# Kernel optimization log

Hardware: AMD Instinct MI355X
Metric: run time of the kernel (lower is better)

The kernel has to match this reference:

```python
import jax, jax.numpy as jnp
import numpy as np

T, B, I, H = 1024, 64, 1024, 1024


def setup_inputs() -> dict:
    key = jax.random.key(0)
    ks = jax.random.split(key, 7)
    s = 1.0 / np.sqrt(H)  # uniform_(-sqrt(k), sqrt(k)) with k = 1/hidden_size
    return {
        "x": jax.random.normal(ks[0], (T, B, I), dtype=jnp.float32),
        "W_ih": jax.random.normal(ks[1], (4 * H, I), dtype=jnp.float32) * s,
        "W_hh": jax.random.normal(ks[2], (4 * H, H), dtype=jnp.float32) * s,
        "b_ih": jax.random.normal(ks[3], (4 * H,), dtype=jnp.float32) * s,
        "b_hh": jax.random.normal(ks[4], (4 * H,), dtype=jnp.float32) * s,
        "h0": jax.random.uniform(ks[5], (B, H), dtype=jnp.float32, minval=-s, maxval=s),
        "c0": jax.random.uniform(ks[6], (B, H), dtype=jnp.float32, minval=-s, maxval=s),
    }


def reference(x, W_ih, W_hh, b_ih, b_hh, h0, c0):
    # Precompute input projections for all timesteps in one big GEMM: [T,B,4H]
    x_proj = jnp.einsum("tbi,gi->tbg", x, W_ih) + b_ih + b_hh

    def step(carry, xp_t):
        h, c = carry
        gates = xp_t + h @ W_hh.T  # [B, 4H]
        i, f, g, o = jnp.split(gates, 4, axis=-1)  # torch LSTMCell gate order
        i = jax.nn.sigmoid(i)
        f = jax.nn.sigmoid(f)
        g = jnp.tanh(g)
        o = jax.nn.sigmoid(o)
        c_new = f * c + i * g
        h_new = o * jnp.tanh(c_new)
        return (h_new, c_new), h_new

    (h_T, c_T), out = jax.lax.scan(step, (h0, c0), x_proj)
    return out, h_T, c_T  # out: [T, B, H]
```

## Files before the change

### kernel.cpp

```cpp
#include <hip/hip_runtime.h>

typedef unsigned short u16;
typedef __attribute__((ext_vector_type(8))) __bf16 bf16x8;
typedef __attribute__((ext_vector_type(4))) float f32x4;

#define NWG 256
#define CHUNK 64
#define NCHUNK 16

__device__ __forceinline__ u16 f2b(float f) {
  union { float f; unsigned u; } v; v.f = f;
  unsigned r = (v.u + 0x7fffu + ((v.u >> 16) & 1u)) >> 16;
  return (u16)r;
}
__device__ __forceinline__ float b2f(u16 u) {
  union { unsigned u; float f; } v; v.u = ((unsigned)u) << 16;
  return v.f;
}
__device__ __forceinline__ float sig(float x) { return 1.0f / (1.0f + __expf(-x)); }
__device__ __forceinline__ float tanh_(float x) { return 2.0f / (1.0f + __expf(-2.0f * x)) - 1.0f; }

__global__ __launch_bounds__(256) void prep_kernel(
    const float* __restrict__ W_ih, const float* __restrict__ W_hh,
    const float* __restrict__ b_ih, const float* __restrict__ b_hh,
    const float* __restrict__ h0, const float* __restrict__ c0,
    u16* __restrict__ Wc, float* __restrict__ bias,
    u16* __restrict__ hbuf, float* __restrict__ cst)
{
  const int tid = threadIdx.x;
  const int blk = blockIdx.x;
  {
    const float4 a = *reinterpret_cast<const float4*>(W_ih + (size_t)blk * 1024 + tid * 4);
    const float4 b = *reinterpret_cast<const float4*>(W_hh + (size_t)blk * 1024 + tid * 4);
    u16* dst = Wc + (size_t)blk * 2048;
    *reinterpret_cast<ushort4*>(dst + tid * 4) =
        make_ushort4(f2b(a.x), f2b(a.y), f2b(a.z), f2b(a.w));
    *reinterpret_cast<ushort4*>(dst + 1024 + tid * 4) =
        make_ushort4(f2b(b.x), f2b(b.y), f2b(b.z), f2b(b.w));
  }
  if (blk < 16) {
    int i = blk * 256 + tid;
    bias[i] = b_ih[i] + b_hh[i];
  } else if (blk < 80) {
    int row = blk - 16, k = tid * 4;
    float4 v = *reinterpret_cast<const float4*>(h0 + (size_t)row * 1024 + k);
    *reinterpret_cast<ushort4*>(hbuf + (size_t)row * 1024 + k) =
        make_ushort4(f2b(v.x), f2b(v.y), f2b(v.z), f2b(v.w));
  } else if (blk < 144) {
    int row = blk - 80, k = tid * 4;
    *reinterpret_cast<float4*>(cst + (size_t)row * 1024 + k) =
        *reinterpret_cast<const float4*>(c0 + (size_t)row * 1024 + k);
  }
}

__global__ __launch_bounds__(256) void xproj_kernel(
    const float* __restrict__ xc, const u16* __restrict__ Wc, u16* __restrict__ Xp)
{
  __shared__ __align__(16) u16 As[128][72];
  __shared__ __align__(16) u16 Bs[128][72];
  const int tid = threadIdx.x;
  const int w = tid >> 6, l = tid & 63;
  const int bm = blockIdx.x & 31;
  const int bn = blockIdx.x >> 5;
  const int m0 = bm << 7, n0 = bn << 7;
  const int wm = w & 1, wn = w >> 1;
  const int lr = l & 15, lq = l >> 4;

  f32x4 acc[4][4];
  for (int i = 0; i < 4; ++i)
    for (int j = 0; j < 4; ++j) acc[i][j] = (f32x4){0.f, 0.f, 0.f, 0.f};

  for (int kc = 0; kc < 1024; kc += 64) {
    {
      const int k4 = (tid & 15) << 2;
      const int rb = tid >> 4;
      for (int rp = 0; rp < 128; rp += 16) {
        int row = rp + rb;
        float4 v = *reinterpret_cast<const float4*>(xc + (size_t)(m0 + row) * 1024 + kc + k4);
        unsigned lo = (unsigned)f2b(v.x) | ((unsigned)f2b(v.y) << 16);
        unsigned hi = (unsigned)f2b(v.z) | ((unsigned)f2b(v.w) << 16);
        *reinterpret_cast<uint2*>(&As[row][k4]) = make_uint2(lo, hi);
      }
    }
    {
      const int kk = (tid & 7) << 3;
      const int rb = tid >> 3;
      for (int rp = 0; rp < 128; rp += 32) {
        int row = rp + rb;
        uint4 v = *reinterpret_cast<const uint4*>(Wc + (size_t)(n0 + row) * 2048 + kc + kk);
        *reinterpret_cast<uint4*>(&Bs[row][kk]) = v;
      }
    }
    __syncthreads();
    for (int kb = 0; kb < 2; ++kb) {
      const int ko = kb * 32 + lq * 8;
      bf16x8 af[4], bfr[4];
      for (int i = 0; i < 4; ++i)
        af[i] = *reinterpret_cast<const bf16x8*>(&As[(wm << 6) + (i << 4) + lr][ko]);
      for (int j = 0; j < 4; ++j)
        bfr[j] = *reinterpret_cast<const bf16x8*>(&Bs[(wn << 6) + (j << 4) + lr][ko]);
      for (int i = 0; i < 4; ++i)
        for (int j = 0; j < 4; ++j)
          acc[i][j] = __builtin_amdgcn_mfma_f32_16x16x32_bf16(af[i], bfr[j], acc[i][j], 0, 0, 0);
    }
    __syncthreads();
  }
  for (int i = 0; i < 4; ++i)
    for (int j = 0; j < 4; ++j) {
      int row0 = m0 + (wm << 6) + (i << 4) + lq * 4;
      int coln = n0 + (wn << 6) + (j << 4) + lr;
      for (int r = 0; r < 4; ++r)
        Xp[(size_t)(row0 + r) * 4096 + coln] = f2b(acc[i][j][r]);
    }
}

__global__ __launch_bounds__(256, 1) void scan_kernel(
    const u16* __restrict__ Wc, const u16* __restrict__ Xp,
    u16* __restrict__ hbuf, float* __restrict__ cst, const float* __restrict__ bias,
    float* __restrict__ out, float* __restrict__ outT, float* __restrict__ cT,
    unsigned* __restrict__ arv, int t0, int C)
{
  __shared__ __align__(16) u16 Wlds[32 * 64 * 8];
  const int tid = threadIdx.x;
  const int g = blockIdx.x;
  const int w = tid >> 6, l = tid & 63;
  const int n = l & 15, kq = l >> 4;
  const int jj = (g << 2) + (n & 3);
  const int col = ((n >> 2) << 10) + jj;

  for (int i = tid; i < 2048; i += 256) {
    int kb = i >> 6, l2 = i & 63;
    int nn = l2 & 15, kq2 = l2 >> 4;
    int c2 = ((nn >> 2) << 10) + (g << 2) + (nn & 3);
    uint4 v = *reinterpret_cast<const uint4*>(Wc + (size_t)c2 * 2048 + 1024 + kb * 32 + kq2 * 8);
    *reinterpret_cast<uint4*>(&Wlds[i * 8]) = v;
  }
  const float biasv = bias[col];
  const int brow = (w << 4) + (kq << 2);
  float creg[4];
  if (n < 4)
    for (int r = 0; r < 4; ++r) creg[r] = cst[(size_t)(brow + r) * 1024 + jj];
  __syncthreads();

  float xv[4];
  {
    const u16* xpr = Xp + ((size_t)brow << 12) + col;
    for (int r = 0; r < 4; ++r) xv[r] = b2f(xpr[(size_t)r << 12]);
  }

  for (int ts = 0; ts < C; ++ts) {
    const int t = t0 + ts;
    const u16* hs = hbuf + ((t & 1) ? 65536 : 0);
    u16* hd = hbuf + ((t & 1) ? 0 : 65536);
    const u16* arow = hs + (size_t)((w << 4) + n) * 1024 + (kq << 3);
    bf16x8 af[32];
#pragma unroll
    for (int kb = 0; kb < 32; ++kb)
      af[kb] = *reinterpret_cast<const bf16x8*>(arow + (kb << 5));
    f32x4 ac0 = {0.f, 0.f, 0.f, 0.f};
    f32x4 ac1 = {0.f, 0.f, 0.f, 0.f};
    f32x4 ac2 = {0.f, 0.f, 0.f, 0.f};
    f32x4 ac3 = {0.f, 0.f, 0.f, 0.f};
#pragma unroll
    for (int kb = 0; kb < 32; kb += 4) {
      ac0 = __builtin_amdgcn_mfma_f32_16x16x32_bf16(
          af[kb + 0], *reinterpret_cast<const bf16x8*>(&Wlds[(((kb + 0) << 6) + l) << 3]), ac0, 0, 0, 0);
      ac1 = __builtin_amdgcn_mfma_f32_16x16x32_bf16(
          af[kb + 1], *reinterpret_cast<const bf16x8*>(&Wlds[(((kb + 1) << 6) + l) << 3]), ac1, 0, 0, 0);
      ac2 = __builtin_amdgcn_mfma_f32_16x16x32_bf16(
          af[kb + 2], *reinterpret_cast<const bf16x8*>(&Wlds[(((kb + 2) << 6) + l) << 3]), ac2, 0, 0, 0);
      ac3 = __builtin_amdgcn_mfma_f32_16x16x32_bf16(
          af[kb + 3], *reinterpret_cast<const bf16x8*>(&Wlds[(((kb + 3) << 6) + l) << 3]), ac3, 0, 0, 0);
    }
    float gv[4];
    for (int r = 0; r < 4; ++r)
      gv[r] = ((ac0[r] + ac1[r]) + (ac2[r] + ac3[r])) + xv[r] + biasv;
    const int sb = (l & 48) | (n & 3);
    float fp[4], gp[4], op[4];
    for (int r = 0; r < 4; ++r) {
      fp[r] = __shfl(gv[r], sb + 4);
      gp[r] = __shfl(gv[r], sb + 8);
      op[r] = __shfl(gv[r], sb + 12);
    }
    float hv[4];
    if (n < 4) {
      for (int r = 0; r < 4; ++r) {
        float iv = sig(gv[r]);
        float fv = sig(fp[r]);
        float gg = tanh_(gp[r]);
        float ov = sig(op[r]);
        float cn = fv * creg[r] + iv * gg;
        hv[r] = ov * tanh_(cn);
        creg[r] = cn;
      }
      unsigned long long pw = (unsigned long long)f2b(hv[0])
                            | ((unsigned long long)f2b(hv[1]) << 16)
                            | ((unsigned long long)f2b(hv[2]) << 32)
                            | ((unsigned long long)f2b(hv[3]) << 48);
      const int tb = l & 48;
      unsigned long long q0 = __shfl(pw, tb + 0);
      unsigned long long q1 = __shfl(pw, tb + 1);
      unsigned long long q2 = __shfl(pw, tb + 2);
      unsigned long long q3 = __shfl(pw, tb + 3);
      const int sh = n << 4;
      unsigned long long st = ((q0 >> sh) & 0xffffull)
                            | (((q1 >> sh) & 0xffffull) << 16)
                            | (((q2 >> sh) & 0xffffull) << 32)
                            | (((q3 >> sh) & 0xffffull) << 48);
      __hip_atomic_store(
          reinterpret_cast<unsigned long long*>(hd + (size_t)(brow + n) * 1024 + (g << 2)),
          st, __ATOMIC_RELAXED, __HIP_MEMORY_SCOPE_AGENT);
    }

    if (ts + 1 < C) {
      const unsigned v = (unsigned)(t + 1);
      __syncthreads();
      if (tid == 0) {
        asm volatile("s_waitcnt vmcnt(0)" ::: "memory");
        __hip_atomic_store(&arv[g << 5], v, __ATOMIC_RELAXED, __HIP_MEMORY_SCOPE_AGENT);
      }
      if (n < 4)
        for (int r = 0; r < 4; ++r)
          __hip_atomic_store(&out[((size_t)t * 64 + (brow + r)) * 1024 + jj], hv[r],
                             __ATOMIC_RELAXED, __HIP_MEMORY_SCOPE_AGENT);
      {
        const u16* xpr = Xp + ((size_t)((ts + 1) * 64 + brow) << 12) + col;
        for (int r = 0; r < 4; ++r) xv[r] = b2f(xpr[(size_t)r << 12]);
      }
      while (__hip_atomic_load(&arv[tid << 5], __ATOMIC_RELAXED, __HIP_MEMORY_SCOPE_AGENT) < v)
        __builtin_amdgcn_s_sleep(1);
      __syncthreads();
      __builtin_amdgcn_fence(__ATOMIC_ACQUIRE, "agent");
    } else {
      if (n < 4)
        for (int r = 0; r < 4; ++r)
          out[((size_t)t * 64 + (brow + r)) * 1024 + jj] = hv[r];
    }
    if (t == 1023 && n < 4)
      for (int r = 0; r < 4; ++r) outT[(size_t)(brow + r) * 1024 + jj] = hv[r];
  }
  if (n < 4) {
    for (int r = 0; r < 4; ++r) cst[(size_t)(brow + r) * 1024 + jj] = creg[r];
    if (t0 + C == 1024)
      for (int r = 0; r < 4; ++r) cT[(size_t)(brow + r) * 1024 + jj] = creg[r];
  }
}

extern "C" void kernel_launch(void* const* d_in, const int* in_sizes, int n_in,
                              void* d_out, int out_size, void* d_ws, size_t ws_size,
                              hipStream_t stream)
{
  const float* x    = (const float*)d_in[0];
  const float* W_ih = (const float*)d_in[1];
  const float* W_hh = (const float*)d_in[2];
  const float* b_ih = (const float*)d_in[3];
  const float* b_hh = (const float*)d_in[4];
  const float* h0   = (const float*)d_in[5];
  const float* c0   = (const float*)d_in[6];
  float* out  = (float*)d_out;
  float* outT = out + (size_t)1024 * 64 * 1024;
  float* cT   = outT + 64 * 1024;

  unsigned char* ws = (unsigned char*)d_ws;
  size_t off = 0;
  u16* Wc = (u16*)(ws + off);      off += (size_t)4096 * 2048 * 2;
  float* bias = (float*)(ws + off); off += 4096 * 4;
  u16* hbuf = (u16*)(ws + off);    off += (size_t)2 * 65536 * 2;
  float* cst = (float*)(ws + off); off += (size_t)65536 * 4;
  unsigned* arv = (unsigned*)(ws + off); off += 256 * 32 * 4;
  u16* Xp = (u16*)(ws + off);

  hipMemsetAsync(arv, 0, 256 * 32 * 4, stream);
  hipLaunchKernelGGL(prep_kernel, dim3(4096), dim3(256), 0, stream,
                     W_ih, W_hh, b_ih, b_hh, h0, c0, Wc, bias, hbuf, cst);

  for (int c = 0; c < NCHUNK; ++c) {
    int t0 = c * CHUNK;
    hipLaunchKernelGGL(xproj_kernel, dim3(1024), dim3(256), 0, stream,
                       x + (size_t)t0 * 65536, Wc, Xp);
    int C = CHUNK;
    void* args[] = {&Wc, &Xp, &hbuf, &cst, &bias, &out, &outT, &cT, &arv, &t0, &C};
    if (hipLaunchCooperativeKernel(reinterpret_cast<void*>(scan_kernel),
                                   dim3(NWG), dim3(256), args, 0, stream) != hipSuccess) {
      (void)hipGetLastError();
      hipLaunchKernelGGL(scan_kernel, dim3(NWG), dim3(256), 0, stream,
                         Wc, Xp, hbuf, cst, bias, out, outT, cT, arv, t0, CHUNK);
    }
  }
}
```

Measured before the change: 16.37 ms.

## Repartition LSTM scan into batch-group tiles with group-local barriers and tiled Xp layout

The scan kernel is re-partitioned so each workgroup owns 16 hidden units across all four gates for a 16-row batch slice. Each wave computes one gate, and the gates are combined through LDS rather than wave shuffles. Workgroups now synchronise only with the 64 members of their own batch group instead of all 256, which is meant to cut grid-wide barrier latency each timestep. The prep GEMM writes Xp in a tiled packed layout so each thread fetches its x-projection with one 8-byte load. In exchange the kernel uses four times the LDS for weights and adds extra __syncthreads per step.

```diff
diff --git a/kernel.cpp b/kernel.cpp
--- a/kernel.cpp
+++ b/kernel.cpp
@@ -105,12 +105,17 @@
     }
     __syncthreads();
   }
+  const int ts2 = (bm << 1) + wm;
+  const int gam = bn >> 3;
   for (int i = 0; i < 4; ++i)
     for (int j = 0; j < 4; ++j) {
-      int row0 = m0 + (wm << 6) + (i << 4) + lq * 4;
-      int coln = n0 + (wn << 6) + (j << 4) + lr;
-      for (int r = 0; r < 4; ++r)
-        Xp[(size_t)(row0 + r) * 4096 + coln] = f2b(acc[i][j][r]);
+      const int q2 = ((bn & 7) << 3) + (wn << 2) + j;
+      unsigned long long pk = (unsigned long long)f2b(acc[i][j][0])
+                            | ((unsigned long long)f2b(acc[i][j][1]) << 16)
+                            | ((unsigned long long)f2b(acc[i][j][2]) << 32)
+                            | ((unsigned long long)f2b(acc[i][j][3]) << 48);
+      size_t off = ((((size_t)(ts2 * 4 + gam) * 64 + q2) * 4 + i) * 16 + lr) * 16 + (lq << 2);
+      *reinterpret_cast<unsigned long long*>(Xp + off) = pk;
     }
 }
 
@@ -120,130 +125,115 @@
     float* __restrict__ out, float* __restrict__ outT, float* __restrict__ cT,
     unsigned* __restrict__ arv, int t0, int C)
 {
-  __shared__ __align__(16) u16 Wlds[32 * 64 * 8];
+  __shared__ __align__(16) u16 Wlds[4 * 32 * 64 * 8];
+  __shared__ __align__(16) float GsF[4 * 16 * 17];
+  __shared__ __align__(8) u16 Hs[256];
   const int tid = threadIdx.x;
-  const int g = blockIdx.x;
+  const int bid = blockIdx.x;
+  const int g = (bid & 7) >> 1;
+  const int q = ((bid >> 3) << 1) | (bid & 1);
   const int w = tid >> 6, l = tid & 63;
-  const int n = l & 15, kq = l >> 4;
-  const int jj = (g << 2) + (n & 3);
-  const int col = ((n >> 2) << 10) + jj;
-
-  for (int i = tid; i < 2048; i += 256) {
-    int kb = i >> 6, l2 = i & 63;
-    int nn = l2 & 15, kq2 = l2 >> 4;
-    int c2 = ((nn >> 2) << 10) + (g << 2) + (nn & 3);
-    uint4 v = *reinterpret_cast<const uint4*>(Wc + (size_t)c2 * 2048 + 1024 + kb * 32 + kq2 * 8);
-    *reinterpret_cast<uint4*>(&Wlds[i * 8]) = v;
-  }
-  const float biasv = bias[col];
-  const int brow = (w << 4) + (kq << 2);
-  float creg[4];
-  if (n < 4)
-    for (int r = 0; r < 4; ++r) creg[r] = cst[(size_t)(brow + r) * 1024 + jj];
+  const int g16 = g << 4, q16 = q << 4;
+  const int member = (g << 6) + q;
+  const int gBase = g << 6;
+
+  for (int it = 0; it < 32; ++it) {
+    int f = it * 256 + tid;
+    int gf = f >> 11, rem = f & 2047;
+    int kb = rem >> 6, lf = rem & 63;
+    int colw = (gf << 10) + q16 + (lf & 15);
+    int k0 = (kb << 5) + ((lf >> 4) << 3);
+    uint4 v = *reinterpret_cast<const uint4*>(Wc + (size_t)colw * 2048 + 1024 + k0);
+    *reinterpret_cast<uint4*>(&Wlds[f * 8]) = v;
+  }
+  const float biasv = bias[(w << 10) + q16 + (l & 15)];
+  const int eb = tid >> 4, ej = tid & 15;
+  float creg = cst[(size_t)(g16 + eb) * 1024 + q16 + ej];
   __syncthreads();
 
   float xv[4];
   {
-    const u16* xpr = Xp + ((size_t)brow << 12) + col;
-    for (int r = 0; r < 4; ++r) xv[r] = b2f(xpr[(size_t)r << 12]);
+    const u16* xp = Xp + (((size_t)(0 * 4 + w) * 64 + q) * 4 + g) * 256
+                    + ((l & 15) << 4) + ((l >> 4) << 2);
+    uint2 xr = *reinterpret_cast<const uint2*>(xp);
+    xv[0] = b2f((u16)(xr.x & 0xffff)); xv[1] = b2f((u16)(xr.x >> 16));
+    xv[2] = b2f((u16)(xr.y & 0xffff)); xv[3] = b2f((u16)(xr.y >> 16));
   }
 
   for (int ts = 0; ts < C; ++ts) {
     const int t = t0 + ts;
     const u16* hs = hbuf + ((t & 1) ? 65536 : 0);
     u16* hd = hbuf + ((t & 1) ? 0 : 65536);
-    const u16* arow = hs + (size_t)((w << 4) + n) * 1024 + (kq << 3);
-    bf16x8 af[32];
-#pragma unroll
-    for (int kb = 0; kb < 32; ++kb)
-      af[kb] = *reinterpret_cast<const bf16x8*>(arow + (kb << 5));
+    const u16* arow = hs + (size_t)(g16 + (l & 15)) * 1024 + ((l >> 4) << 3);
     f32x4 ac0 = {0.f, 0.f, 0.f, 0.f};
     f32x4 ac1 = {0.f, 0.f, 0.f, 0.f};
-    f32x4 ac2 = {0.f, 0.f, 0.f, 0.f};
-    f32x4 ac3 = {0.f, 0.f, 0.f, 0.f};
 #pragma unroll
-    for (int kb = 0; kb < 32; kb += 4) {
+    for (int kb = 0; kb < 32; kb += 2) {
+      bf16x8 a0 = *reinterpret_cast<const bf16x8*>(arow + (kb << 5));
+      bf16x8 a1 = *reinterpret_cast<const bf16x8*>(arow + ((kb + 1) << 5));
       ac0 = __builtin_amdgcn_mfma_f32_16x16x32_bf16(
-          af[kb + 0], *reinterpret_cast<const bf16x8*>(&Wlds[(((kb + 0) << 6) + l) << 3]), ac0, 0, 0, 0);
+          a0, *reinterpret_cast<const bf16x8*>(&Wlds[(((w << 5) + kb) * 64 + l) * 8]), ac0, 0, 0, 0);
       ac1 = __builtin_amdgcn_mfma_f32_16x16x32_bf16(
-          af[kb + 1], *reinterpret_cast<const bf16x8*>(&Wlds[(((kb + 1) << 6) + l) << 3]), ac1, 0, 0, 0);
-      ac2 = __builtin_amdgcn_mfma_f32_16x16x32_bf16(
-          af[kb + 2], *reinterpret_cast<const bf16x8*>(&Wlds[(((kb + 2) << 6) + l) << 3]), ac2, 0, 0, 0);
-      ac3 = __builtin_amdgcn_mfma_f32_16x16x32_bf16(
-          af[kb + 3], *reinterpret_cast<const bf16x8*>(&Wlds[(((kb + 3) << 6) + l) << 3]), ac3, 0, 0, 0);
-    }
-    float gv[4];
-    for (int r = 0; r < 4; ++r)
-      gv[r] = ((ac0[r] + ac1[r]) + (ac2[r] + ac3[r])) + xv[r] + biasv;
-    const int sb = (l & 48) | (n & 3);
-    float fp[4], gp[4], op[4];
+          a1, *reinterpret_cast<const bf16x8*>(&Wlds[(((w << 5) + kb + 1) * 64 + l) * 8]), ac1, 0, 0, 0);
+    }
+#pragma unroll
     for (int r = 0; r < 4; ++r) {
-      fp[r] = __shfl(gv[r], sb + 4);
-      gp[r] = __shfl(gv[r], sb + 8);
-      op[r] = __shfl(gv[r], sb + 12);
-    }
-    float hv[4];
-    if (n < 4) {
-      for (int r = 0; r < 4; ++r) {
-        float iv = sig(gv[r]);
-        float fv = sig(fp[r]);
-        float gg = tanh_(gp[r]);
-        float ov = sig(op[r]);
-        float cn = fv * creg[r] + iv * gg;
-        hv[r] = ov * tanh_(cn);
-        creg[r] = cn;
-      }
-      unsigned long long pw = (unsigned long long)f2b(hv[0])
-                            | ((unsigned long long)f2b(hv[1]) << 16)
-                            | ((unsigned long long)f2b(hv[2]) << 32)
-                            | ((unsigned long long)f2b(hv[3]) << 48);
-      const int tb = l & 48;
-      unsigned long long q0 = __shfl(pw, tb + 0);
-      unsigned long long q1 = __shfl(pw, tb + 1);
-      unsigned long long q2 = __shfl(pw, tb + 2);
-      unsigned long long q3 = __shfl(pw, tb + 3);
-      const int sh = n << 4;
-      unsigned long long st = ((q0 >> sh) & 0xffffull)
-                            | (((q1 >> sh) & 0xffffull) << 16)
-                            | (((q2 >> sh) & 0xffffull) << 32)
-                            | (((q3 >> sh) & 0xffffull) << 48);
-      __hip_atomic_store(
-          reinterpret_cast<unsigned long long*>(hd + (size_t)(brow + n) * 1024 + (g << 2)),
-          st, __ATOMIC_RELAXED, __HIP_MEMORY_SCOPE_AGENT);
-    }
+      float val = (ac0[r] + ac1[r]) + xv[r] + biasv;
+      GsF[((w << 4) + ((l >> 4) << 2) + r) * 17 + (l & 15)] = val;
+    }
+    __syncthreads();
+    float gi = sig(GsF[(0 * 16 + eb) * 17 + ej]);
+    float gf_ = sig(GsF[(1 * 16 + eb) * 17 + ej]);
+    float gg = tanh_(GsF[(2 * 16 + eb) * 17 + ej]);
+    float go = sig(GsF[(3 * 16 + eb) * 17 + ej]);
+    float cn = gf_ * creg + gi * gg;
+    float hv = go * tanh_(cn);
+    creg = cn;
+    Hs[tid] = f2b(hv);
+    if (ts + 1 < C) {
+      const u16* xp = Xp + (((size_t)((ts + 1) * 4 + w) * 64 + q) * 4 + g) * 256
+                      + ((l & 15) << 4) + ((l >> 4) << 2);
+      uint2 xr = *reinterpret_cast<const uint2*>(xp);
+      xv[0] = b2f((u16)(xr.x & 0xffff)); xv[1] = b2f((u16)(xr.x >> 16));
+      xv[2] = b2f((u16)(xr.y & 0xffff)); xv[3] = b2f((u16)(xr.y >> 16));
+    }
+    __syncthreads();
 
     if (ts + 1 < C) {
       const unsigned v = (unsigned)(t + 1);
-      __syncthreads();
-      if (tid == 0) {
-        asm volatile("s_waitcnt vmcnt(0)" ::: "memory");
-        __hip_atomic_store(&arv[g << 5], v, __ATOMIC_RELAXED, __HIP_MEMORY_SCOPE_AGENT);
-      }
-      if (n < 4)
-        for (int r = 0; r < 4; ++r)
-          __hip_atomic_store(&out[((size_t)t * 64 + (brow + r)) * 1024 + jj], hv[r],
-                             __ATOMIC_RELAXED, __HIP_MEMORY_SCOPE_AGENT);
-      {
-        const u16* xpr = Xp + ((size_t)((ts + 1) * 64 + brow) << 12) + col;
-        for (int r = 0; r < 4; ++r) xv[r] = b2f(xpr[(size_t)r << 12]);
-      }
-      while (__hip_atomic_load(&arv[tid << 5], __ATOMIC_RELAXED, __HIP_MEMORY_SCOPE_AGENT) < v)
-        __builtin_amdgcn_s_sleep(1);
+      if (tid < 64) {
+        unsigned long long st =
+            *reinterpret_cast<const unsigned long long*>(&Hs[((tid >> 2) << 4) + ((tid & 3) << 2)]);
+        __hip_atomic_store(
+            reinterpret_cast<unsigned long long*>(
+                hd + (size_t)(g16 + (tid >> 2)) * 1024 + q16 + ((tid & 3) << 2)),
+            st, __ATOMIC_RELAXED, __HIP_MEMORY_SCOPE_AGENT);
+        if (tid == 0) {
+          asm volatile("s_waitcnt vmcnt(0)" ::: "memory");
+          __hip_atomic_store(&arv[member << 5], v, __ATOMIC_RELAXED, __HIP_MEMORY_SCOPE_AGENT);
+        }
+      }
+      __hip_atomic_store(&out[((size_t)t * 64 + g16 + eb) * 1024 + q16 + ej], hv,
+                         __ATOMIC_RELAXED, __HIP_MEMORY_SCOPE_AGENT);
+      if (tid < 64)
+        while (__hip_atomic_load(&arv[(gBase + tid) << 5], __ATOMIC_RELAXED,
+                                 __HIP_MEMORY_SCOPE_AGENT) < v)
+          __builtin_amdgcn_s_sleep(1);
       __syncthreads();
       __builtin_amdgcn_fence(__ATOMIC_ACQUIRE, "agent");
     } else {
-      if (n < 4)
-        for (int r = 0; r < 4; ++r)
-          out[((size_t)t * 64 + (brow + r)) * 1024 + jj] = hv[r];
-    }
-    if (t == 1023 && n < 4)
-      for (int r = 0; r < 4; ++r) outT[(size_t)(brow + r) * 1024 + jj] = hv[r];
-  }
-  if (n < 4) {
-    for (int r = 0; r < 4; ++r) cst[(size_t)(brow + r) * 1024 + jj] = creg[r];
-    if (t0 + C == 1024)
-      for (int r = 0; r < 4; ++r) cT[(size_t)(brow + r) * 1024 + jj] = creg[r];
-  }
+      if (tid < 64) {
+        unsigned long long st =
+            *reinterpret_cast<const unsigned long long*>(&Hs[((tid >> 2) << 4) + ((tid & 3) << 2)]);
+        *reinterpret_cast<unsigned long long*>(
+            hd + (size_t)(g16 + (tid >> 2)) * 1024 + q16 + ((tid & 3) << 2)) = st;
+      }
+      out[((size_t)t * 64 + g16 + eb) * 1024 + q16 + ej] = hv;
+      if (t == 1023) outT[(size_t)(g16 + eb) * 1024 + q16 + ej] = hv;
+    }
+  }
+  cst[(size_t)(g16 + eb) * 1024 + q16 + ej] = creg;
+  if (t0 + C == 1024) cT[(size_t)(g16 + eb) * 1024 + q16 + ej] = creg;
 }
 
 extern "C" void kernel_launch(void* const* d_in, const int* in_sizes, int n_in,
```

Result: faster. 14.82 ms (-9.4%).
